# Performance work log

Hardware: AMD Instinct MI355X
Metric: run time of the kernel (lower is better)

Reference implementation:

```python
import jax, jax.numpy as jnp
import numpy as np

B, S, D, H, FF = 2, 2048, 1024, 16, 4096
HD = D // H
EPS = 1e-9


def setup_inputs() -> dict:
    key = jax.random.key(0)
    ks = jax.random.split(key, 16)
    sc = 0.02
    inp = {
        "x": jax.random.normal(ks[0], (B, S, D), jnp.float32),
        "y": jax.random.normal(ks[1], (B, S, D), jnp.float32),
        "decoder_mask": jnp.tril(jnp.ones((S, S), jnp.int32))[None, None],  # [1,1,S,S]
        # self-attention params (weights stored [in,out])
        "qkv_w": jax.random.normal(ks[2], (D, 3 * D), jnp.float32) * sc,
        "qkv_b": jnp.zeros((3 * D,), jnp.float32),
        "sa_fc_w": jax.random.normal(ks[3], (D, D), jnp.float32) * sc,
        "sa_fc_b": jnp.zeros((D,), jnp.float32),
        "g1": jnp.ones((D,), jnp.float32),
        "b1": jnp.zeros((D,), jnp.float32),
        # cross-attention params
        "kv_w": jax.random.normal(ks[4], (D, 2 * D), jnp.float32) * sc,
        "kv_b": jnp.zeros((2 * D,), jnp.float32),
        "q_w": jax.random.normal(ks[5], (D, D), jnp.float32) * sc,
        "q_b": jnp.zeros((D,), jnp.float32),
        "ca_fc_w": jax.random.normal(ks[6], (D, D), jnp.float32) * sc,
        "ca_fc_b": jnp.zeros((D,), jnp.float32),
        "g2": jnp.ones((D,), jnp.float32),
        "b2": jnp.zeros((D,), jnp.float32),
        # FFN params
        "ff1_w": jax.random.normal(ks[7], (D, FF), jnp.float32) * sc,
        "ff1_b": jnp.zeros((FF,), jnp.float32),
        "ff2_w": jax.random.normal(ks[8], (FF, D), jnp.float32) * sc,
        "ff2_b": jnp.zeros((D,), jnp.float32),
        "g3": jnp.ones((D,), jnp.float32),
        "b3": jnp.zeros((D,), jnp.float32),
    }
    return inp


def _layernorm(x, g, b):
    mean = jnp.mean(x, axis=-1, keepdims=True)
    var = jnp.mean((x - mean) ** 2, axis=-1, keepdims=True)
    return g * (x - mean) / jnp.sqrt(var + EPS) + b


def _sdpa(q, k, v, mask=None):
    # q,k,v: [B,H,S,hd]
    scores = jnp.einsum("bhqd,bhkd->bhqk", q, k) / jnp.sqrt(jnp.float32(q.shape[-1]))
    if mask is not None:
        scores = jnp.where(mask == 0, jnp.float32(-1e9), scores)
    attn = jax.nn.softmax(scores, axis=-1)
    return jnp.einsum("bhqk,bhkd->bhqd", attn, v)


def reference(x, y, decoder_mask, qkv_w, qkv_b, sa_fc_w, sa_fc_b, g1, b1,
              kv_w, kv_b, q_w, q_b, ca_fc_w, ca_fc_b, g2, b2,
              ff1_w, ff1_b, ff2_w, ff2_b, g3, b3):
    b, s, d = y.shape
    # --- masked self-attention on y ---
    qkv = (y @ qkv_w + qkv_b).reshape(b, s, H, 3 * HD).transpose(0, 2, 1, 3)
    q, k, v = jnp.split(qkv, 3, axis=-1)
    vals = _sdpa(q, k, v, decoder_mask).transpose(0, 2, 1, 3).reshape(b, s, d)
    sa = vals @ sa_fc_w + sa_fc_b
    y = _layernorm(sa + y, g1, b1)
    # --- cross-attention: kv from x, q from y ---
    kv = (x @ kv_w + kv_b).reshape(b, s, H, 2 * HD).transpose(0, 2, 1, 3)
    k2, v2 = jnp.split(kv, 2, axis=-1)
    q2 = (y @ q_w + q_b).reshape(b, s, H, HD).transpose(0, 2, 1, 3)
    vals2 = _sdpa(q2, k2, v2, None).transpose(0, 2, 1, 3).reshape(b, s, d)
    ca = vals2 @ ca_fc_w + ca_fc_b
    y = _layernorm(ca + y, g2, b2)
    # --- FFN ---
    h = jax.nn.relu(y @ ff1_w + ff1_b)
    ff = h @ ff2_w + ff2_b
    y = _layernorm(ff + y, g3, b3)
    return y
```

## Files before the change

### kernel.cpp

```cpp
#include <hip/hip_runtime.h>

typedef unsigned short u16;
typedef unsigned int u32;
typedef __attribute__((ext_vector_type(4))) float f32x4;
typedef __attribute__((ext_vector_type(8))) __bf16 bf16x8;
typedef __attribute__((ext_vector_type(2))) __bf16 bf16x2;
typedef __attribute__((ext_vector_type(4))) u16 u16x4;

#define NB 2
#define NS 2048
#define ND 1024
#define NH 16
#define NHD 64
#define NFF 4096
#define NBS (NB * NS)

typedef const __attribute__((address_space(1))) unsigned int as1_u32;
typedef __attribute__((address_space(3))) unsigned int as3_u32;

__device__ __forceinline__ void gl_lds16(const u16* g, u16* l) {
  __builtin_amdgcn_global_load_lds((as1_u32*)g, (as3_u32*)l, 16, 0, 0);
}

__device__ __forceinline__ u16 f2bf(float f) {
  union { float f; unsigned u; } v; v.f = f;
  unsigned r = (v.u + 0x7FFFu + ((v.u >> 16) & 1u)) >> 16;
  return (u16)r;
}

__device__ __forceinline__ float bf2f(u16 u) {
  union { u32 u; float f; } v; v.u = ((u32)u) << 16; return v.f;
}

__device__ __forceinline__ u32 pkbf(float a, float b) {
  bf16x2 v; v[0] = (__bf16)a; v[1] = (__bf16)b;
  union { bf16x2 v; u32 u; } c; c.v = v; return c.u;
}

__device__ __forceinline__ char* lswz(void* base, int row, int bcol) {
  return (char*)base + row * 128 + (bcol ^ ((row & 7) << 4));
}
__device__ __forceinline__ const char* lswz(const void* base, int row, int bcol) {
  return (const char*)base + row * 128 + (bcol ^ ((row & 7) << 4));
}

__global__ __launch_bounds__(256) void conv_bf16(const float* __restrict__ in,
                                                 u16* __restrict__ out, int n4) {
  int i = blockIdx.x * 256 + threadIdx.x;
  if (i >= n4) return;
  f32x4 v = *reinterpret_cast<const f32x4*>(&in[(size_t)i * 4]);
  u16x4 o;
#pragma unroll
  for (int j = 0; j < 4; ++j) o[j] = f2bf(v[j]);
  *reinterpret_cast<u16x4*>(&out[(size_t)i * 4]) = o;
}

__global__ void wconv_t(const float* __restrict__ in, u16* __restrict__ out, int K, int N) {
  __shared__ float t[32][33];
  int n0 = blockIdx.x * 32, k0 = blockIdx.y * 32;
  int tx = threadIdx.x, ty = threadIdx.y;
#pragma unroll
  for (int i = ty; i < 32; i += 8) t[i][tx] = in[(size_t)(k0 + i) * N + n0 + tx];
  __syncthreads();
#pragma unroll
  for (int i = ty; i < 32; i += 8)
    out[(size_t)(n0 + i) * K + k0 + tx] = f2bf(t[tx][i]);
}

template <int TM, int OUTF32, int RELU>
__global__ __launch_bounds__(256) void gemm_bt(const u16* __restrict__ A,
                                               const u16* __restrict__ BT,
                                               const float* __restrict__ bias,
                                               float* __restrict__ Cf,
                                               u16* __restrict__ Cb,
                                               int M, int N, int K) {
  constexpr int MR = TM / 32;
  constexpr int ACH = TM / 64;
  __shared__ __align__(16) u16 lA[2][TM * 32];
  __shared__ __align__(16) u16 lB[2][128 * 32];
  const int tid = threadIdx.x;
  const int lane = tid & 63, wave = tid >> 6;
  const int bm = blockIdx.y * TM, bn = blockIdx.x * 128;
  const int wr = (wave >> 1) * (MR * 16), wc = (wave & 1) * 64;
  const int r16 = lane & 15, kg = lane >> 4;

  f32x4 acc[MR][4] = {};

  auto stage = [&](int buf, int k0) {
#pragma unroll
    for (int c = 0; c < ACH; ++c) {
      int chunk = c * 256 + tid;
      int r = chunk >> 2, kc = (chunk & 3) * 8;
      gl_lds16(&A[(size_t)(bm + r) * K + k0 + kc], &lA[buf][(c * 256 + wave * 64) * 8]);
    }
#pragma unroll
    for (int c = 0; c < 2; ++c) {
      int chunk = c * 256 + tid;
      int r = chunk >> 2, kc = (chunk & 3) * 8;
      gl_lds16(&BT[(size_t)(bn + r) * K + k0 + kc], &lB[buf][(c * 256 + wave * 64) * 8]);
    }
  };

  stage(0, 0);
  __syncthreads();

  const int nk = K / 32;
  for (int i = 0; i < nk; ++i) {
    const int cur = i & 1;
    if (i + 1 < nk) stage(cur ^ 1, (i + 1) * 32);

    bf16x8 af[MR], bfr[4];
#pragma unroll
    for (int m = 0; m < MR; ++m)
      af[m] = *reinterpret_cast<const bf16x8*>(&lA[cur][(wr + m * 16 + r16) * 32 + kg * 8]);
#pragma unroll
    for (int n = 0; n < 4; ++n)
      bfr[n] = *reinterpret_cast<const bf16x8*>(&lB[cur][(wc + n * 16 + r16) * 32 + kg * 8]);
#pragma unroll
    for (int m = 0; m < MR; ++m)
#pragma unroll
      for (int n = 0; n < 4; ++n)
        acc[m][n] = __builtin_amdgcn_mfma_f32_16x16x32_bf16(af[m], bfr[n], acc[m][n], 0, 0, 0);

    __syncthreads();
  }

#pragma unroll
  for (int m = 0; m < MR; ++m) {
    int row = bm + wr + m * 16 + kg * 4;
#pragma unroll
    for (int n = 0; n < 4; ++n) {
      int col = bn + wc + n * 16 + r16;
      float bv = bias[col];
#pragma unroll
      for (int j = 0; j < 4; ++j) {
        float v = acc[m][n][j] + bv;
        if (RELU) v = fmaxf(v, 0.f);
        if (OUTF32)
          Cf[(size_t)(row + j) * N + col] = v;
        else
          Cb[(size_t)(row + j) * N + col] = f2bf(v);
      }
    }
  }
}

__global__ __launch_bounds__(256) void vt_kern(const u16* __restrict__ src, int stride,
                                               int hmul, int hadd, u16* __restrict__ VT) {
  __shared__ u16 lt[64][72];
  const int bh = blockIdx.y;
  const int b = bh >> 4, h = bh & 15;
  const int s0 = blockIdx.x * 64;
  const u16* sb = src + (size_t)b * NS * stride + h * hmul + hadd;
#pragma unroll
  for (int c = 0; c < 2; ++c) {
    int chunk = c * 256 + threadIdx.x;
    int r = chunk >> 3, d = (chunk & 7) * 8;
    *reinterpret_cast<uint4*>(&lt[r][d]) =
        *reinterpret_cast<const uint4*>(&sb[(size_t)(s0 + r) * stride + d]);
  }
  __syncthreads();
  const int d = threadIdx.x >> 2, sq = (threadIdx.x & 3) * 16;
  union { u16 e[16]; uint4 v[2]; } pk;
#pragma unroll
  for (int i = 0; i < 16; ++i) pk.e[i] = lt[sq + i][d];
  uint4* dst = reinterpret_cast<uint4*>(&VT[((size_t)bh * NHD + d) * NS + s0 + sq]);
  dst[0] = pk.v[0];
  dst[1] = pk.v[1];
}

#define C1F 0.180336880f
#define OPSZ ((size_t)32 * NS * NHD)

template <int CAUSAL>
__global__ __launch_bounds__(256) void attn8(const u16* __restrict__ Qp, int qstride,
                                             int qhm, const u16* __restrict__ Kp,
                                             int kstride, int khm, int kha,
                                             const u16* __restrict__ VT,
                                             u16* __restrict__ OP,
                                             float2* __restrict__ ML) {
  const int bid = blockIdx.x;
  const int split = blockIdx.y;
  const int xcd = bid & 7, j5 = bid >> 3;
  const int bh = xcd + 8 * (j5 >> 4);
  int qt = j5 & 15;
  if (CAUSAL) qt = 15 - qt;
  const int b = bh >> 4, h = bh & 15;
  const int tid = threadIdx.x, lane = tid & 63, wave = tid >> 6;
  const int r16 = lane & 15, kg = lane >> 4;
  const int q0w = qt * 128 + wave * 32;

  __shared__ __align__(16) char lK[2][64 * 128];
  __shared__ __align__(16) char lV[2][64 * 128];
  __shared__ __align__(16) char lP[4][32 * 128];
  char* lPw = &lP[wave][0];

  const u16* qb = Qp + (size_t)b * NS * qstride + h * qhm;
  const u16* kb = Kp + (size_t)b * NS * kstride + h * khm + kha;
  const u16* vb = VT + (size_t)bh * NHD * NS;

  const int srow = tid >> 3;
  const int sbcol = (tid & 7) * 16;
  const int scol = (tid & 7) * 8;

  bf16x8 qf[2][2];
#pragma unroll
  for (int qn = 0; qn < 2; ++qn)
#pragma unroll
    for (int ks = 0; ks < 2; ++ks)
      qf[qn][ks] = *reinterpret_cast<const bf16x8*>(
          &qb[(size_t)(q0w + qn * 16 + r16) * qstride + ks * 32 + kg * 8]);

  f32x4 o_acc[2][4] = {};
  float m_run[2] = {-1e30f, -1e30f}, l_lane[2] = {0.f, 0.f};

  const int ntb = CAUSAL ? (2 * qt + 2) : (NS / 64);
  const int wnt = CAUSAL ? (q0w / 64 + 1) : (NS / 64);
  const int halfb = (ntb + 1) >> 1;
  const int t0 = split ? halfb : 0;
  const int t1 = split ? ntb : halfb;

  uint4 kreg[2], vreg[2];
  auto ldregs = [&](int t) {
    const int kv0 = t * 64;
#pragma unroll
    for (int c = 0; c < 2; ++c) {
      kreg[c] = *reinterpret_cast<const uint4*>(
          &kb[(size_t)(kv0 + srow + c * 32) * kstride + scol]);
      vreg[c] = *reinterpret_cast<const uint4*>(
          &vb[(size_t)(srow + c * 32) * NS + kv0 + scol]);
    }
  };
  auto wrlds = [&](int buf) {
#pragma unroll
    for (int c = 0; c < 2; ++c) {
      *reinterpret_cast<uint4*>(lswz(lK[buf], srow + c * 32, sbcol)) = kreg[c];
      *reinterpret_cast<uint4*>(lswz(lV[buf], srow + c * 32, sbcol)) = vreg[c];
    }
  };

  ldregs(t0);
  wrlds(0);
  __syncthreads();

  for (int t = t0; t < t1; ++t) {
    const int cur = (t - t0) & 1;
    const bool more = (t + 1 < t1);
    if (more) ldregs(t + 1);

    if (t < wnt) {
      const int kv0 = t * 64;
      const char* lKc = lK[cur];
      const char* lVc = lV[cur];

      bf16x8 kf[8];
#pragma unroll
      for (int c = 0; c < 4; ++c)
#pragma unroll
        for (int ks = 0; ks < 2; ++ks)
          kf[c * 2 + ks] = *reinterpret_cast<const bf16x8*>(
              lswz(lKc, c * 16 + r16, ks * 64 + kg * 16));

      f32x4 s[2][4] = {};
#pragma unroll
      for (int c = 0; c < 4; ++c)
#pragma unroll
        for (int ks = 0; ks < 2; ++ks) {
          s[0][c] = __builtin_amdgcn_mfma_f32_16x16x32_bf16(kf[c * 2 + ks], qf[0][ks], s[0][c], 0, 0, 0);
          s[1][c] = __builtin_amdgcn_mfma_f32_16x16x32_bf16(kf[c * 2 + ks], qf[1][ks], s[1][c], 0, 0, 0);
        }

      bf16x8 vf[8];
#pragma unroll
      for (int cd = 0; cd < 4; ++cd)
#pragma unroll
        for (int ks = 0; ks < 2; ++ks)
          vf[cd * 2 + ks] = *reinterpret_cast<const bf16x8*>(
              lswz(lVc, cd * 16 + r16, ks * 64 + kg * 16));

#pragma unroll
      for (int qn = 0; qn < 2; ++qn) {
        if (CAUSAL && t == wnt - 1) {
          const int q = q0w + qn * 16 + r16;
#pragma unroll
          for (int c = 0; c < 4; ++c)
#pragma unroll
            for (int j = 0; j < 4; ++j)
              if (kv0 + c * 16 + kg * 4 + j > q) s[qn][c][j] = -1e31f;
        }
        float mxr = s[qn][0][0];
#pragma unroll
        for (int c = 0; c < 4; ++c)
#pragma unroll
          for (int j = 0; j < 4; ++j) mxr = fmaxf(mxr, s[qn][c][j]);
        float mn = m_run[qn];
        if (!__all(mxr * C1F <= mn + 8.f)) {
          float mz = mxr * C1F;
          mz = fmaxf(mz, __shfl_xor(mz, 16));
          mz = fmaxf(mz, __shfl_xor(mz, 32));
          mn = fmaxf(m_run[qn], mz);
          const float cr = exp2f(m_run[qn] - mn);
          m_run[qn] = mn;
          l_lane[qn] *= cr;
          float crow[4];
#pragma unroll
          for (int j = 0; j < 4; ++j) crow[j] = __shfl(cr, kg * 4 + j);
#pragma unroll
          for (int cd = 0; cd < 4; ++cd)
#pragma unroll
            for (int j = 0; j < 4; ++j) o_acc[qn][cd][j] *= crow[j];
        }
        float su = 0.f;
#pragma unroll
        for (int c = 0; c < 4; ++c)
#pragma unroll
          for (int j = 0; j < 4; ++j) {
            float p = exp2f(fmaf(s[qn][c][j], C1F, -mn));
            s[qn][c][j] = p;
            su += p;
          }
        l_lane[qn] += su;

#pragma unroll
        for (int c = 0; c < 4; ++c) {
          uint2 w2 = {pkbf(s[qn][c][0], s[qn][c][1]), pkbf(s[qn][c][2], s[qn][c][3])};
          *reinterpret_cast<uint2*>(lswz(lPw, qn * 16 + r16, c * 32 + kg * 8)) = w2;
        }
      }

      bf16x8 pf[2][2];
#pragma unroll
      for (int qn = 0; qn < 2; ++qn)
#pragma unroll
        for (int ks = 0; ks < 2; ++ks)
          pf[qn][ks] = *reinterpret_cast<const bf16x8*>(
              lswz(lPw, qn * 16 + r16, ks * 64 + kg * 16));
#pragma unroll
      for (int cd = 0; cd < 4; ++cd)
#pragma unroll
        for (int ks = 0; ks < 2; ++ks) {
          o_acc[0][cd] = __builtin_amdgcn_mfma_f32_16x16x32_bf16(pf[0][ks], vf[cd * 2 + ks],
                                                                 o_acc[0][cd], 0, 0, 0);
          o_acc[1][cd] = __builtin_amdgcn_mfma_f32_16x16x32_bf16(pf[1][ks], vf[cd * 2 + ks],
                                                                 o_acc[1][cd], 0, 0, 0);
        }
    }

    if (more) wrlds(cur ^ 1);
    __syncthreads();
  }

  u16* op = OP + split * OPSZ + (size_t)bh * NS * NHD;
#pragma unroll
  for (int qn = 0; qn < 2; ++qn) {
    float l = l_lane[qn];
    l += __shfl_xor(l, 16);
    l += __shfl_xor(l, 32);
#pragma unroll
    for (int cd = 0; cd < 4; ++cd) {
      int col = cd * 16 + r16;
#pragma unroll
      for (int j = 0; j < 4; ++j) {
        int row = q0w + qn * 16 + kg * 4 + j;
        op[(size_t)row * NHD + col] = f2bf(o_acc[qn][cd][j]);
      }
    }
    if (kg == 0)
      ML[(size_t)split * 32 * NS + (size_t)bh * NS + q0w + qn * 16 + r16] =
          make_float2(m_run[qn], l);
  }
}

__global__ __launch_bounds__(256) void attn_comb(const u16* __restrict__ OP,
                                                 const float2* __restrict__ ML,
                                                 u16* __restrict__ AO) {
  int idx = blockIdx.x * 256 + threadIdx.x;
  int dg = (idx & 7) * 8;
  int q = (idx >> 3) & (NS - 1);
  int bh = idx >> 14;
  int b = bh >> 4, h = bh & 15;
  float2 ml0 = ML[(size_t)bh * NS + q];
  float2 ml1 = ML[(size_t)32 * NS + (size_t)bh * NS + q];
  float M = fmaxf(ml0.x, ml1.x);
  float w0 = exp2f(ml0.x - M), w1 = exp2f(ml1.x - M);
  float linv = 1.f / (ml0.y * w0 + ml1.y * w1);
  w0 *= linv;
  w1 *= linv;
  size_t src = ((size_t)bh * NS + q) * NHD + dg;
  uint4 r0 = *reinterpret_cast<const uint4*>(&OP[src]);
  uint4 r1 = *reinterpret_cast<const uint4*>(&OP[OPSZ + src]);
  const u16* e0 = reinterpret_cast<const u16*>(&r0);
  const u16* e1 = reinterpret_cast<const u16*>(&r1);
  u16 out[8];
#pragma unroll
  for (int j = 0; j < 8; ++j)
    out[j] = f2bf(bf2f(e0[j]) * w0 + bf2f(e1[j]) * w1);
  *reinterpret_cast<uint4*>(&AO[((size_t)b * NS + q) * ND + h * NHD + dg]) =
      *reinterpret_cast<uint4*>(out);
}

__global__ __launch_bounds__(256) void ln_kern(const float* __restrict__ a,
                                               const float* __restrict__ resid,
                                               const float* __restrict__ g,
                                               const float* __restrict__ bb,
                                               float* __restrict__ outf,
                                               u16* __restrict__ outb) {
  const int row = blockIdx.x;
  const int tid = threadIdx.x;
  const size_t off = (size_t)row * ND + tid * 4;
  f32x4 v = *reinterpret_cast<const f32x4*>(&a[off]);
  f32x4 r = *reinterpret_cast<const f32x4*>(&resid[off]);
#pragma unroll
  for (int j = 0; j < 4; ++j) v[j] += r[j];
  float s = v[0] + v[1] + v[2] + v[3];
  float s2 = v[0] * v[0] + v[1] * v[1] + v[2] * v[2] + v[3] * v[3];
#pragma unroll
  for (int m = 1; m < 64; m <<= 1) {
    s += __shfl_xor(s, m);
    s2 += __shfl_xor(s2, m);
  }
  __shared__ float ws1[4], ws2[4];
  int wave = tid >> 6, lane = tid & 63;
  if (lane == 0) { ws1[wave] = s; ws2[wave] = s2; }
  __syncthreads();
  s = ws1[0] + ws1[1] + ws1[2] + ws1[3];
  s2 = ws2[0] + ws2[1] + ws2[2] + ws2[3];
  float mean = s * (1.f / ND);
  float var = fmaxf(s2 * (1.f / ND) - mean * mean, 0.f);
  float rstd = rsqrtf(var + 1e-9f);
  f32x4 gg = *reinterpret_cast<const f32x4*>(&g[tid * 4]);
  f32x4 bv = *reinterpret_cast<const f32x4*>(&bb[tid * 4]);
  f32x4 o;
  u16x4 ob;
#pragma unroll
  for (int j = 0; j < 4; ++j) {
    o[j] = gg[j] * (v[j] - mean) * rstd + bv[j];
    ob[j] = f2bf(o[j]);
  }
  *reinterpret_cast<f32x4*>(&outf[off]) = o;
  *reinterpret_cast<u16x4*>(&outb[off]) = ob;
}

extern "C" void kernel_launch(void* const* d_in, const int* in_sizes, int n_in,
                              void* d_out, int out_size, void* d_ws, size_t ws_size,
                              hipStream_t stream) {
  const float* x = (const float*)d_in[0];
  const float* y = (const float*)d_in[1];
  const float* qkv_w = (const float*)d_in[3];
  const float* qkv_b = (const float*)d_in[4];
  const float* sa_fc_w = (const float*)d_in[5];
  const float* sa_fc_b = (const float*)d_in[6];
  const float* g1 = (const float*)d_in[7];
  const float* b1 = (const float*)d_in[8];
  const float* kv_w = (const float*)d_in[9];
  const float* kv_b = (const float*)d_in[10];
  const float* q_w = (const float*)d_in[11];
  const float* q_b = (const float*)d_in[12];
  const float* ca_fc_w = (const float*)d_in[13];
  const float* ca_fc_b = (const float*)d_in[14];
  const float* g2 = (const float*)d_in[15];
  const float* b2 = (const float*)d_in[16];
  const float* ff1_w = (const float*)d_in[17];
  const float* ff1_b = (const float*)d_in[18];
  const float* ff2_w = (const float*)d_in[19];
  const float* ff2_b = (const float*)d_in[20];
  const float* g3 = (const float*)d_in[21];
  const float* b3 = (const float*)d_in[22];

  if (ws_size < (120ull << 20)) return;

  char* w = (char*)d_ws;
  u16* W16 = (u16*)(w + 0);
  u16* ACT = (u16*)(w + (8ull << 20));
  u16* XB  = (u16*)(w + (16ull << 20));
  u16* Qb  = (u16*)(w + (24ull << 20));
  u16* VT  = (u16*)(w + (40ull << 20));
  u16* AO  = (u16*)(w + (48ull << 20));
  u16* G   = (u16*)(w + (56ull << 20));
  float* Fa = (float*)(w + (88ull << 20));
  float* Fb = (float*)(w + (104ull << 20));
  u16* OPb = ACT;
  float2* ML = (float2*)w;
  float* OUT = (float*)d_out;

  dim3 wblk(32, 8);
  const int n4act = NBS * ND / 4;

  conv_bf16<<<n4act / 256, 256, 0, stream>>>(y, ACT, n4act);
  wconv_t<<<dim3(3 * ND / 32, ND / 32), wblk, 0, stream>>>(qkv_w, W16, ND, 3 * ND);
  gemm_bt<128, 0, 0><<<dim3(3 * ND / 128, NBS / 128), 256, 0, stream>>>(
      ACT, W16, qkv_b, nullptr, G, NBS, 3 * ND, ND);
  vt_kern<<<dim3(NS / 64, NB * NH), 256, 0, stream>>>(G, 3 * ND, 192, 128, VT);
  attn8<1><<<dim3(512, 2), 256, 0, stream>>>(G, 3 * ND, 192, G, 3 * ND, 192, 64, VT, OPb, ML);
  attn_comb<<<2048, 256, 0, stream>>>(OPb, ML, AO);
  wconv_t<<<dim3(ND / 32, ND / 32), wblk, 0, stream>>>(sa_fc_w, W16, ND, ND);
  gemm_bt<64, 1, 0><<<dim3(ND / 128, NBS / 64), 256, 0, stream>>>(
      AO, W16, sa_fc_b, Fa, nullptr, NBS, ND, ND);
  ln_kern<<<NBS, 256, 0, stream>>>(Fa, y, g1, b1, Fb, ACT);

  conv_bf16<<<n4act / 256, 256, 0, stream>>>(x, XB, n4act);
  wconv_t<<<dim3(2 * ND / 32, ND / 32), wblk, 0, stream>>>(kv_w, W16, ND, 2 * ND);
  gemm_bt<128, 0, 0><<<dim3(2 * ND / 128, NBS / 128), 256, 0, stream>>>(
      XB, W16, kv_b, nullptr, G, NBS, 2 * ND, ND);
  vt_kern<<<dim3(NS / 64, NB * NH), 256, 0, stream>>>(G, 2 * ND, 128, 64, VT);
  wconv_t<<<dim3(ND / 32, ND / 32), wblk, 0, stream>>>(q_w, W16, ND, ND);
  gemm_bt<64, 0, 0><<<dim3(ND / 128, NBS / 64), 256, 0, stream>>>(
      ACT, W16, q_b, nullptr, Qb, NBS, ND, ND);
  attn8<0><<<dim3(512, 2), 256, 0, stream>>>(Qb, ND, 64, G, 2 * ND, 128, 0, VT, OPb, ML);
  attn_comb<<<2048, 256, 0, stream>>>(OPb, ML, AO);
  wconv_t<<<dim3(ND / 32, ND / 32), wblk, 0, stream>>>(ca_fc_w, W16, ND, ND);
  gemm_bt<64, 1, 0><<<dim3(ND / 128, NBS / 64), 256, 0, stream>>>(
      AO, W16, ca_fc_b, Fa, nullptr, NBS, ND, ND);
  ln_kern<<<NBS, 256, 0, stream>>>(Fa, Fb, g2, b2, Fb, ACT);

  wconv_t<<<dim3(NFF / 32, ND / 32), wblk, 0, stream>>>(ff1_w, W16, ND, NFF);
  gemm_bt<128, 0, 1><<<dim3(NFF / 128, NBS / 128), 256, 0, stream>>>(
      ACT, W16, ff1_b, nullptr, G, NBS, NFF, ND);
  wconv_t<<<dim3(ND / 32, NFF / 32), wblk, 0, stream>>>(ff2_w, W16, NFF, ND);
  gemm_bt<64, 1, 0><<<dim3(ND / 128, NBS / 64), 256, 0, stream>>>(
      G, W16, ff2_b, Fa, nullptr, NBS, ND, NFF);
  ln_kern<<<NBS, 256, 0, stream>>>(Fa, Fb, g3, b3, OUT, ACT);
}
```

Before: 518.1 us.

## Enlarge attention query tile to 256 rows with 8 waves, prescale Q

The attention kernel now runs 512 threads (8 waves) per block covering 256 query rows, so each K/V tile staged in LDS is shared by twice as many waves and each thread loads half as much per tile. The grid is halved to 256x2 blocks. Q is also pre-multiplied by the softmax scale constant when loaded, which removes a multiply from the max and exp path. Costs are fewer blocks in flight, coarser causal work balance, and a small extra rounding from scaling Q in bf16.

```diff
diff --git a/kernel.cpp b/kernel.cpp
--- a/kernel.cpp
+++ b/kernel.cpp
@@ -173,7 +173,7 @@
 #define OPSZ ((size_t)32 * NS * NHD)
 
 template <int CAUSAL>
-__global__ __launch_bounds__(256) void attn8(const u16* __restrict__ Qp, int qstride,
+__global__ __launch_bounds__(512) void attn9(const u16* __restrict__ Qp, int qstride,
                                              int qhm, const u16* __restrict__ Kp,
                                              int kstride, int khm, int kha,
                                              const u16* __restrict__ VT,
@@ -182,17 +182,17 @@
   const int bid = blockIdx.x;
   const int split = blockIdx.y;
   const int xcd = bid & 7, j5 = bid >> 3;
-  const int bh = xcd + 8 * (j5 >> 4);
-  int qt = j5 & 15;
-  if (CAUSAL) qt = 15 - qt;
+  const int bh = xcd + 8 * (j5 >> 3);
+  int qt = j5 & 7;
+  if (CAUSAL) qt = 7 - qt;
   const int b = bh >> 4, h = bh & 15;
   const int tid = threadIdx.x, lane = tid & 63, wave = tid >> 6;
   const int r16 = lane & 15, kg = lane >> 4;
-  const int q0w = qt * 128 + wave * 32;
+  const int q0w = qt * 256 + wave * 32;
 
   __shared__ __align__(16) char lK[2][64 * 128];
   __shared__ __align__(16) char lV[2][64 * 128];
-  __shared__ __align__(16) char lP[4][32 * 128];
+  __shared__ __align__(16) char lP[8][32 * 128];
   char* lPw = &lP[wave][0];
 
   const u16* qb = Qp + (size_t)b * NS * qstride + h * qhm;
@@ -207,36 +207,32 @@
 #pragma unroll
   for (int qn = 0; qn < 2; ++qn)
 #pragma unroll
-    for (int ks = 0; ks < 2; ++ks)
-      qf[qn][ks] = *reinterpret_cast<const bf16x8*>(
+    for (int ks = 0; ks < 2; ++ks) {
+      bf16x8 v = *reinterpret_cast<const bf16x8*>(
           &qb[(size_t)(q0w + qn * 16 + r16) * qstride + ks * 32 + kg * 8]);
+#pragma unroll
+      for (int e = 0; e < 8; ++e) v[e] = (__bf16)((float)v[e] * C1F);
+      qf[qn][ks] = v;
+    }
 
   f32x4 o_acc[2][4] = {};
   float m_run[2] = {-1e30f, -1e30f}, l_lane[2] = {0.f, 0.f};
 
-  const int ntb = CAUSAL ? (2 * qt + 2) : (NS / 64);
+  const int ntb = CAUSAL ? (4 * qt + 4) : (NS / 64);
   const int wnt = CAUSAL ? (q0w / 64 + 1) : (NS / 64);
   const int halfb = (ntb + 1) >> 1;
   const int t0 = split ? halfb : 0;
   const int t1 = split ? ntb : halfb;
 
-  uint4 kreg[2], vreg[2];
+  uint4 kreg, vreg;
   auto ldregs = [&](int t) {
     const int kv0 = t * 64;
-#pragma unroll
-    for (int c = 0; c < 2; ++c) {
-      kreg[c] = *reinterpret_cast<const uint4*>(
-          &kb[(size_t)(kv0 + srow + c * 32) * kstride + scol]);
-      vreg[c] = *reinterpret_cast<const uint4*>(
-          &vb[(size_t)(srow + c * 32) * NS + kv0 + scol]);
-    }
+    kreg = *reinterpret_cast<const uint4*>(&kb[(size_t)(kv0 + srow) * kstride + scol]);
+    vreg = *reinterpret_cast<const uint4*>(&vb[(size_t)srow * NS + kv0 + scol]);
   };
   auto wrlds = [&](int buf) {
-#pragma unroll
-    for (int c = 0; c < 2; ++c) {
-      *reinterpret_cast<uint4*>(lswz(lK[buf], srow + c * 32, sbcol)) = kreg[c];
-      *reinterpret_cast<uint4*>(lswz(lV[buf], srow + c * 32, sbcol)) = vreg[c];
-    }
+    *reinterpret_cast<uint4*>(lswz(lK[buf], srow, sbcol)) = kreg;
+    *reinterpret_cast<uint4*>(lswz(lV[buf], srow, sbcol)) = vreg;
   };
 
   ldregs(t0);
@@ -288,14 +284,14 @@
             for (int j = 0; j < 4; ++j)
               if (kv0 + c * 16 + kg * 4 + j > q) s[qn][c][j] = -1e31f;
         }
-        float mxr = s[qn][0][0];
-#pragma unroll
-        for (int c = 0; c < 4; ++c)
-#pragma unroll
-          for (int j = 0; j < 4; ++j) mxr = fmaxf(mxr, s[qn][c][j]);
+        float m0 = fmaxf(fmaxf(s[qn][0][0], s[qn][0][1]), fmaxf(s[qn][0][2], s[qn][0][3]));
+        float m1 = fmaxf(fmaxf(s[qn][1][0], s[qn][1][1]), fmaxf(s[qn][1][2], s[qn][1][3]));
+        float m2 = fmaxf(fmaxf(s[qn][2][0], s[qn][2][1]), fmaxf(s[qn][2][2], s[qn][2][3]));
+        float m3 = fmaxf(fmaxf(s[qn][3][0], s[qn][3][1]), fmaxf(s[qn][3][2], s[qn][3][3]));
+        float mxr = fmaxf(fmaxf(m0, m1), fmaxf(m2, m3));
         float mn = m_run[qn];
-        if (!__all(mxr * C1F <= mn + 8.f)) {
-          float mz = mxr * C1F;
+        if (!__all(mxr <= mn + 8.f)) {
+          float mz = mxr;
           mz = fmaxf(mz, __shfl_xor(mz, 16));
           mz = fmaxf(mz, __shfl_xor(mz, 32));
           mn = fmaxf(m_run[qn], mz);
@@ -315,7 +311,7 @@
         for (int c = 0; c < 4; ++c)
 #pragma unroll
           for (int j = 0; j < 4; ++j) {
-            float p = exp2f(fmaf(s[qn][c][j], C1F, -mn));
+            float p = exp2f(s[qn][c][j] - mn);
             s[qn][c][j] = p;
             su += p;
           }
@@ -491,7 +487,7 @@
   gemm_bt<128, 0, 0><<<dim3(3 * ND / 128, NBS / 128), 256, 0, stream>>>(
       ACT, W16, qkv_b, nullptr, G, NBS, 3 * ND, ND);
   vt_kern<<<dim3(NS / 64, NB * NH), 256, 0, stream>>>(G, 3 * ND, 192, 128, VT);
-  attn8<1><<<dim3(512, 2), 256, 0, stream>>>(G, 3 * ND, 192, G, 3 * ND, 192, 64, VT, OPb, ML);
+  attn9<1><<<dim3(256, 2), 512, 0, stream>>>(G, 3 * ND, 192, G, 3 * ND, 192, 64, VT, OPb, ML);
   attn_comb<<<2048, 256, 0, stream>>>(OPb, ML, AO);
   wconv_t<<<dim3(ND / 32, ND / 32), wblk, 0, stream>>>(sa_fc_w, W16, ND, ND);
   gemm_bt<64, 1, 0><<<dim3(ND / 128, NBS / 64), 256, 0, stream>>>(
@@ -506,7 +502,7 @@
   wconv_t<<<dim3(ND / 32, ND / 32), wblk, 0, stream>>>(q_w, W16, ND, ND);
   gemm_bt<64, 0, 0><<<dim3(ND / 128, NBS / 64), 256, 0, stream>>>(
       ACT, W16, q_b, nullptr, Qb, NBS, ND, ND);
-  attn8<0><<<dim3(512, 2), 256, 0, stream>>>(Qb, ND, 64, G, 2 * ND, 128, 0, VT, OPb, ML);
+  attn9<0><<<dim3(256, 2), 512, 0, stream>>>(Qb, ND, 64, G, 2 * ND, 128, 0, VT, OPb, ML);
   attn_comb<<<2048, 256, 0, stream>>>(OPb, ML, AO);
   wconv_t<<<dim3(ND / 32, ND / 32), wblk, 0, stream>>>(ca_fc_w, W16, ND, ND);
   gemm_bt<64, 1, 0><<<dim3(ND / 128, NBS / 64), 256, 0, stream>>>(
```

Result: faster. 467.2 us (-9.8%).
